# Optimization experiments

Measured on AMD Instinct MI355X. Metric: run time of the kernel, lower is better.

The kernel has to match this reference:

```python
import jax, jax.numpy as jnp
import numpy as np

G = 2000      # num_genes
TF = 64       # num_tf
B = 32        # batch (cells)
_peaks = 5 + (np.arange(G) % 46)          # ragged peaks per gene, avg ~27
T = int(_peaks.sum())                      # 54736 total peak columns
E = G * 16                                 # directed edges before symmetrization


def setup_inputs() -> dict:
    key = jax.random.key(0)
    ks = jax.random.split(key, 8)
    x = jax.random.normal(ks[0], (B, TF, T), jnp.float32)
    # gene id of each peak column (sorted, ragged segment structure = cut[])
    gene_ids = jnp.asarray(np.repeat(np.arange(G), _peaks), jnp.int32)
    # all per-gene subNet Linear weights flattened into one [TF, T] table
    w_sub = jax.random.normal(ks[1], (TF, T), jnp.float32) * 0.02
    b_sub = jax.random.normal(ks[2], (G,), jnp.float32) * 0.02
    rng = np.random.default_rng(1)
    src = rng.integers(0, G, E)
    dst = rng.integers(0, G, E)
    ei = np.stack([np.concatenate([src, dst]), np.concatenate([dst, src])])
    edge_index = jnp.asarray(ei, jnp.int32)                 # [2, 2E], symmetrized
    w_conv = jax.random.normal(ks[3], (1, 2), jnp.float32) * 0.5   # GCN lin weight (in=1, out=2)
    b_conv = jax.random.normal(ks[4], (2,), jnp.float32) * 0.1
    w_out = jax.random.normal(ks[5], (G * 2, 3), jnp.float32) * 0.02
    b_out = jax.random.normal(ks[6], (3,), jnp.float32) * 0.02
    return dict(x=x, gene_ids=gene_ids, w_sub=w_sub, b_sub=b_sub,
                edge_index=edge_index, w_conv=w_conv, b_conv=b_conv,
                w_out=w_out, b_out=b_out)


def reference(x, gene_ids, w_sub, b_sub, edge_index, w_conv, b_conv, w_out, b_out):
    # --- ragged per-gene subNets: Linear(num_peak_i*TF, 1) each ---
    # out[b,g] = sum_{t, p in gene g} x[b,t,p] * w[g,t,p] + b_sub[g]
    z = (x * w_sub[None]).sum(axis=1)                        # [B, T] reduce over TF
    x_cat = jnp.zeros((x.shape[0], b_sub.shape[0]), x.dtype)
    x_cat = x_cat.at[:, gene_ids].add(z) + b_sub[None]       # segment-sum over peaks
    x_cat = jax.nn.relu(x_cat)                               # cat_activate

    # --- GCNConv(1, 2, add_self_loops=False) on node features [B, G, 1] ---
    h = jnp.einsum('bn,f->bnf', x_cat, w_conv[0])            # lin: [B, G, 2]
    src, dst = edge_index[0], edge_index[1]
    deg = jnp.zeros((b_sub.shape[0],), x.dtype).at[dst].add(1.0)
    dinv = jnp.where(deg > 0, jax.lax.rsqrt(jnp.maximum(deg, 1.0)), 0.0)
    norm = dinv[src] * dinv[dst]                             # [2E]
    msg = h[:, src, :] * norm[None, :, None]                 # gather + scale
    agg = jnp.zeros_like(h).at[:, dst, :].add(msg) + b_conv  # scatter-add + bias
    g = jax.nn.relu(agg).reshape(x.shape[0], -1)             # [B, G*2]

    out = g @ w_out + b_out                                   # [B, 3]
    return x_cat, g, out
```

## Files before the change

### kernel.cpp

```cpp
#include <hip/hip_runtime.h>


__global__ void k_subnet(const float* __restrict__ x, const float* __restrict__ w_sub,
                         const int* __restrict__ gene_ids, float* __restrict__ acc,
                         int TF, int T, int G) {
    int t = (blockIdx.x * blockDim.x + threadIdx.x) * 4;
    int b = blockIdx.y;
    if (t >= T) return;
    const size_t xbase = (size_t)b * TF * T;
    if (t + 3 < T && (T % 4) == 0) {
        const float4* xp = (const float4*)(x + xbase + t);
        const float4* wp = (const float4*)(w_sub + t);
        const size_t strideV = (size_t)T / 4;
        float4 a = make_float4(0.f, 0.f, 0.f, 0.f);
        #pragma unroll 8
        for (int tf = 0; tf < TF; ++tf) {
            float4 xv = xp[(size_t)tf * strideV];
            float4 wv = wp[(size_t)tf * strideV];
            a.x += xv.x * wv.x;
            a.y += xv.y * wv.y;
            a.z += xv.z * wv.z;
            a.w += xv.w * wv.w;
        }
        int g0 = gene_ids[t], g1 = gene_ids[t + 1], g2 = gene_ids[t + 2], g3 = gene_ids[t + 3];
        float* base = acc + (size_t)b * G;
        float v = a.x; int cg = g0;
        if (g1 == cg) v += a.y; else { atomicAdd(base + cg, v); cg = g1; v = a.y; }
        if (g2 == cg) v += a.z; else { atomicAdd(base + cg, v); cg = g2; v = a.z; }
        if (g3 == cg) v += a.w; else { atomicAdd(base + cg, v); cg = g3; v = a.w; }
        atomicAdd(base + cg, v);
    } else {
        for (int tt = t; tt < T && tt < t + 4; ++tt) {
            float a = 0.f;
            for (int tf = 0; tf < TF; ++tf)
                a += x[xbase + (size_t)tf * T + tt] * w_sub[(size_t)tf * T + tt];
            atomicAdd(acc + (size_t)b * G + gene_ids[tt], a);
        }
    }
}

__global__ void k_xcat(const float* __restrict__ acc, const float* __restrict__ b_sub,
                       float* __restrict__ xcat, int BG, int G) {
    int i = blockIdx.x * blockDim.x + threadIdx.x;
    if (i >= BG) return;
    int g = i % G;
    float v = acc[i] + b_sub[g];
    xcat[i] = v > 0.f ? v : 0.f;
}

__global__ void k_deg(const int* __restrict__ ei, float* __restrict__ deg, int E2) {
    int e = blockIdx.x * blockDim.x + threadIdx.x;
    if (e < E2) atomicAdd(&deg[ei[E2 + e]], 1.0f);
}

__global__ void k_dinv(float* __restrict__ deg, int G) {
    int g = blockIdx.x * blockDim.x + threadIdx.x;
    if (g < G) {
        float d = deg[g];
        deg[g] = (d > 0.f) ? (1.0f / sqrtf(fmaxf(d, 1.0f))) : 0.f;
    }
}

__global__ void k_scatter(const float* __restrict__ xcat, const int* __restrict__ ei,
                          const float* __restrict__ dinv, float* __restrict__ s,
                          int G, int E2, int total) {
    int idx = blockIdx.x * blockDim.x + threadIdx.x;
    if (idx >= total) return;
    int b = idx / E2;
    int e = idx - b * E2;
    int src = ei[e], dst = ei[E2 + e];
    float norm = dinv[src] * dinv[dst];
    atomicAdd(&s[(size_t)b * G + dst], xcat[(size_t)b * G + src] * norm);
}

__global__ void k_gfin(const float* __restrict__ s, const float* __restrict__ w_conv,
                       const float* __restrict__ b_conv, float* __restrict__ gout, int BG) {
    int i = blockIdx.x * blockDim.x + threadIdx.x;
    if (i >= BG) return;
    float sv = s[i];
    float g0 = sv * w_conv[0] + b_conv[0];
    float g1 = sv * w_conv[1] + b_conv[1];
    gout[2 * (size_t)i + 0] = g0 > 0.f ? g0 : 0.f;
    gout[2 * (size_t)i + 1] = g1 > 0.f ? g1 : 0.f;
}

__global__ void k_out(const float* __restrict__ gmat, const float* __restrict__ w_out,
                      const float* __restrict__ b_out, float* __restrict__ out, int G2) {
    int b = blockIdx.x;
    float a0 = 0.f, a1 = 0.f, a2 = 0.f;
    for (int i = threadIdx.x; i < G2; i += blockDim.x) {
        float gv = gmat[(size_t)b * G2 + i];
        a0 += gv * w_out[3 * i + 0];
        a1 += gv * w_out[3 * i + 1];
        a2 += gv * w_out[3 * i + 2];
    }
    __shared__ float red[3][256];
    red[0][threadIdx.x] = a0; red[1][threadIdx.x] = a1; red[2][threadIdx.x] = a2;
    __syncthreads();
    for (int s = blockDim.x / 2; s > 0; s >>= 1) {
        if ((int)threadIdx.x < s) {
            red[0][threadIdx.x] += red[0][threadIdx.x + s];
            red[1][threadIdx.x] += red[1][threadIdx.x + s];
            red[2][threadIdx.x] += red[2][threadIdx.x + s];
        }
        __syncthreads();
    }
    if (threadIdx.x == 0) {
        out[b * 3 + 0] = red[0][0] + b_out[0];
        out[b * 3 + 1] = red[1][0] + b_out[1];
        out[b * 3 + 2] = red[2][0] + b_out[2];
    }
}

extern "C" void kernel_launch(void* const* d_in, const int* in_sizes, int n_in,
                              void* d_out, int out_size, void* d_ws, size_t ws_size,
                              hipStream_t stream) {
    const float* x        = (const float*)d_in[0];
    const int*   gene_ids = (const int*)d_in[1];
    const float* w_sub    = (const float*)d_in[2];
    const float* b_sub    = (const float*)d_in[3];
    const int*   ei       = (const int*)d_in[4];
    const float* w_conv   = (const float*)d_in[5];
    const float* b_conv   = (const float*)d_in[6];
    const float* w_out    = (const float*)d_in[7];
    const float* b_out    = (const float*)d_in[8];

    const int G  = in_sizes[3];
    const int T  = in_sizes[1];
    const int TF = in_sizes[2] / T;
    const int B  = in_sizes[0] / (TF * T);
    const int E2 = in_sizes[4] / 2;
    const int BG = B * G;
    const int G2 = 2 * G;

    float* acc = (float*)d_ws;
    float* deg = acc + BG;
    float* s   = deg + G;
    size_t zero_bytes = (size_t)(BG + G + BG) * sizeof(float);
    hipMemsetAsync(d_ws, 0, zero_bytes, stream);

    float* out_xcat = (float*)d_out;
    float* out_g    = out_xcat + BG;
    float* out_fin  = out_g + (size_t)B * G2;

    {
        int tthreads = (T + 3) / 4;
        dim3 grid((tthreads + 255) / 256, B);
        k_subnet<<<grid, 256, 0, stream>>>(x, w_sub, gene_ids, acc, TF, T, G);
    }
    k_xcat<<<(BG + 255) / 256, 256, 0, stream>>>(acc, b_sub, out_xcat, BG, G);
    k_deg<<<(E2 + 255) / 256, 256, 0, stream>>>(ei, deg, E2);
    k_dinv<<<(G + 255) / 256, 256, 0, stream>>>(deg, G);
    {
        int total = B * E2;
        k_scatter<<<(total + 255) / 256, 256, 0, stream>>>(out_xcat, ei, deg, s, G, E2, total);
    }
    k_gfin<<<(BG + 255) / 256, 256, 0, stream>>>(s, w_conv, b_conv, out_g, BG);
    k_out<<<B, 256, 0, stream>>>(out_g, w_out, b_out, out_fin, G2);
}
```

Baseline: 740.4 us.

## Fuse small GCN kernels, inline rsqrt norm, use nontemporal x loads

Merges xcat, degree counting and output-bias init into one kernel, folds the dinv computation into the scatter kernel, and fuses the gfin and final matvec into one kernel that reduces with wave shuffles and atomics. The subnet kernel now uses nontemporal vector loads for x and a single int4 load for gene ids. The aim is to cut launch count and intermediate round trips. In exchange it recomputes rsqrt per edge per batch and adds atomics on the output.

```diff
diff --git a/kernel.cpp b/kernel.cpp
--- a/kernel.cpp
+++ b/kernel.cpp
@@ -1,5 +1,7 @@
 #include <hip/hip_runtime.h>
 
+
+typedef float f32x4 __attribute__((ext_vector_type(4)));
 
 __global__ void k_subnet(const float* __restrict__ x, const float* __restrict__ w_sub,
                          const int* __restrict__ gene_ids, float* __restrict__ acc,
@@ -9,25 +11,22 @@
     if (t >= T) return;
     const size_t xbase = (size_t)b * TF * T;
     if (t + 3 < T && (T % 4) == 0) {
-        const float4* xp = (const float4*)(x + xbase + t);
-        const float4* wp = (const float4*)(w_sub + t);
+        const f32x4* xp = (const f32x4*)(x + xbase + t);
+        const f32x4* wp = (const f32x4*)(w_sub + t);
         const size_t strideV = (size_t)T / 4;
-        float4 a = make_float4(0.f, 0.f, 0.f, 0.f);
+        f32x4 a = {0.f, 0.f, 0.f, 0.f};
         #pragma unroll 8
         for (int tf = 0; tf < TF; ++tf) {
-            float4 xv = xp[(size_t)tf * strideV];
-            float4 wv = wp[(size_t)tf * strideV];
-            a.x += xv.x * wv.x;
-            a.y += xv.y * wv.y;
-            a.z += xv.z * wv.z;
-            a.w += xv.w * wv.w;
+            f32x4 xv = __builtin_nontemporal_load(xp + (size_t)tf * strideV);
+            f32x4 wv = wp[(size_t)tf * strideV];
+            a += xv * wv;
         }
-        int g0 = gene_ids[t], g1 = gene_ids[t + 1], g2 = gene_ids[t + 2], g3 = gene_ids[t + 3];
+        int4 gi = *(const int4*)(gene_ids + t);
         float* base = acc + (size_t)b * G;
-        float v = a.x; int cg = g0;
-        if (g1 == cg) v += a.y; else { atomicAdd(base + cg, v); cg = g1; v = a.y; }
-        if (g2 == cg) v += a.z; else { atomicAdd(base + cg, v); cg = g2; v = a.z; }
-        if (g3 == cg) v += a.w; else { atomicAdd(base + cg, v); cg = g3; v = a.w; }
+        float v = a.x; int cg = gi.x;
+        if (gi.y == cg) v += a.y; else { atomicAdd(base + cg, v); cg = gi.y; v = a.y; }
+        if (gi.z == cg) v += a.z; else { atomicAdd(base + cg, v); cg = gi.z; v = a.z; }
+        if (gi.w == cg) v += a.w; else { atomicAdd(base + cg, v); cg = gi.w; v = a.w; }
         atomicAdd(base + cg, v);
     } else {
         for (int tt = t; tt < T && tt < t + 4; ++tt) {
@@ -39,76 +38,66 @@
     }
 }
 
-__global__ void k_xcat(const float* __restrict__ acc, const float* __restrict__ b_sub,
-                       float* __restrict__ xcat, int BG, int G) {
+__global__ void k_xcatdeg(const float* __restrict__ acc, const float* __restrict__ b_sub,
+                          float* __restrict__ xcat,
+                          const int* __restrict__ ei, float* __restrict__ deg,
+                          const float* __restrict__ b_out, float* __restrict__ out_fin,
+                          int BG, int G, int E2, int B3) {
     int i = blockIdx.x * blockDim.x + threadIdx.x;
-    if (i >= BG) return;
-    int g = i % G;
-    float v = acc[i] + b_sub[g];
-    xcat[i] = v > 0.f ? v : 0.f;
-}
-
-__global__ void k_deg(const int* __restrict__ ei, float* __restrict__ deg, int E2) {
-    int e = blockIdx.x * blockDim.x + threadIdx.x;
-    if (e < E2) atomicAdd(&deg[ei[E2 + e]], 1.0f);
-}
-
-__global__ void k_dinv(float* __restrict__ deg, int G) {
-    int g = blockIdx.x * blockDim.x + threadIdx.x;
-    if (g < G) {
-        float d = deg[g];
-        deg[g] = (d > 0.f) ? (1.0f / sqrtf(fmaxf(d, 1.0f))) : 0.f;
+    if (i < BG) {
+        int g = i % G;
+        float v = acc[i] + b_sub[g];
+        xcat[i] = v > 0.f ? v : 0.f;
     }
+    if (i < E2) atomicAdd(&deg[ei[E2 + i]], 1.0f);
+    if (i < B3) out_fin[i] = b_out[i % 3];
 }
 
 __global__ void k_scatter(const float* __restrict__ xcat, const int* __restrict__ ei,
-                          const float* __restrict__ dinv, float* __restrict__ s,
-                          int G, int E2, int total) {
-    int idx = blockIdx.x * blockDim.x + threadIdx.x;
-    if (idx >= total) return;
-    int b = idx / E2;
-    int e = idx - b * E2;
+                          const float* __restrict__ deg, float* __restrict__ s,
+                          int G, int E2) {
+    int e = blockIdx.x * blockDim.x + threadIdx.x;
+    if (e >= E2) return;
+    int b = blockIdx.y;
     int src = ei[e], dst = ei[E2 + e];
-    float norm = dinv[src] * dinv[dst];
-    atomicAdd(&s[(size_t)b * G + dst], xcat[(size_t)b * G + src] * norm);
+    float ds = deg[src], dd = deg[dst];
+    float ns = (ds > 0.f) ? (1.0f / sqrtf(fmaxf(ds, 1.0f))) : 0.f;
+    float nd = (dd > 0.f) ? (1.0f / sqrtf(fmaxf(dd, 1.0f))) : 0.f;
+    atomicAdd(&s[(size_t)b * G + dst], xcat[(size_t)b * G + src] * (ns * nd));
 }
 
-__global__ void k_gfin(const float* __restrict__ s, const float* __restrict__ w_conv,
-                       const float* __restrict__ b_conv, float* __restrict__ gout, int BG) {
-    int i = blockIdx.x * blockDim.x + threadIdx.x;
-    if (i >= BG) return;
-    float sv = s[i];
-    float g0 = sv * w_conv[0] + b_conv[0];
-    float g1 = sv * w_conv[1] + b_conv[1];
-    gout[2 * (size_t)i + 0] = g0 > 0.f ? g0 : 0.f;
-    gout[2 * (size_t)i + 1] = g1 > 0.f ? g1 : 0.f;
-}
-
-__global__ void k_out(const float* __restrict__ gmat, const float* __restrict__ w_out,
-                      const float* __restrict__ b_out, float* __restrict__ out, int G2) {
-    int b = blockIdx.x;
+__global__ void k_gfinout(const float* __restrict__ s, const float* __restrict__ w_conv,
+                          const float* __restrict__ b_conv, const float* __restrict__ w_out,
+                          float* __restrict__ gout, float* __restrict__ out_fin, int G) {
+    int n = blockIdx.x * blockDim.x + threadIdx.x;
+    int b = blockIdx.y;
     float a0 = 0.f, a1 = 0.f, a2 = 0.f;
-    for (int i = threadIdx.x; i < G2; i += blockDim.x) {
-        float gv = gmat[(size_t)b * G2 + i];
-        a0 += gv * w_out[3 * i + 0];
-        a1 += gv * w_out[3 * i + 1];
-        a2 += gv * w_out[3 * i + 2];
+    if (n < G) {
+        size_t i = (size_t)b * G + n;
+        float sv = s[i];
+        float g0 = sv * w_conv[0] + b_conv[0]; g0 = g0 > 0.f ? g0 : 0.f;
+        float g1 = sv * w_conv[1] + b_conv[1]; g1 = g1 > 0.f ? g1 : 0.f;
+        gout[2 * i + 0] = g0;
+        gout[2 * i + 1] = g1;
+        const float* w0 = w_out + (size_t)6 * n;
+        a0 = g0 * w0[0] + g1 * w0[3];
+        a1 = g0 * w0[1] + g1 * w0[4];
+        a2 = g0 * w0[2] + g1 * w0[5];
     }
-    __shared__ float red[3][256];
-    red[0][threadIdx.x] = a0; red[1][threadIdx.x] = a1; red[2][threadIdx.x] = a2;
+    for (int off = 32; off > 0; off >>= 1) {
+        a0 += __shfl_down(a0, off);
+        a1 += __shfl_down(a1, off);
+        a2 += __shfl_down(a2, off);
+    }
+    __shared__ float red[3][4];
+    int lane = threadIdx.x & 63;
+    int wid  = threadIdx.x >> 6;
+    if (lane == 0) { red[0][wid] = a0; red[1][wid] = a1; red[2][wid] = a2; }
     __syncthreads();
-    for (int s = blockDim.x / 2; s > 0; s >>= 1) {
-        if ((int)threadIdx.x < s) {
-            red[0][threadIdx.x] += red[0][threadIdx.x + s];
-            red[1][threadIdx.x] += red[1][threadIdx.x + s];
-            red[2][threadIdx.x] += red[2][threadIdx.x + s];
-        }
-        __syncthreads();
-    }
     if (threadIdx.x == 0) {
-        out[b * 3 + 0] = red[0][0] + b_out[0];
-        out[b * 3 + 1] = red[1][0] + b_out[1];
-        out[b * 3 + 2] = red[2][0] + b_out[2];
+        atomicAdd(&out_fin[b * 3 + 0], red[0][0] + red[0][1] + red[0][2] + red[0][3]);
+        atomicAdd(&out_fin[b * 3 + 1], red[1][0] + red[1][1] + red[1][2] + red[1][3]);
+        atomicAdd(&out_fin[b * 3 + 2], red[2][0] + red[2][1] + red[2][2] + red[2][3]);
     }
 }
 
@@ -131,30 +120,34 @@
     const int B  = in_sizes[0] / (TF * T);
     const int E2 = in_sizes[4] / 2;
     const int BG = B * G;
-    const int G2 = 2 * G;
 
     float* acc = (float*)d_ws;
     float* deg = acc + BG;
     float* s   = deg + G;
-    size_t zero_bytes = (size_t)(BG + G + BG) * sizeof(float);
-    hipMemsetAsync(d_ws, 0, zero_bytes, stream);
+    hipMemsetAsync(d_ws, 0, (size_t)(BG + G + BG) * sizeof(float), stream);
 
     float* out_xcat = (float*)d_out;
     float* out_g    = out_xcat + BG;
-    float* out_fin  = out_g + (size_t)B * G2;
+    float* out_fin  = out_g + (size_t)2 * BG;
 
     {
         int tthreads = (T + 3) / 4;
         dim3 grid((tthreads + 255) / 256, B);
         k_subnet<<<grid, 256, 0, stream>>>(x, w_sub, gene_ids, acc, TF, T, G);
     }
-    k_xcat<<<(BG + 255) / 256, 256, 0, stream>>>(acc, b_sub, out_xcat, BG, G);
-    k_deg<<<(E2 + 255) / 256, 256, 0, stream>>>(ei, deg, E2);
-    k_dinv<<<(G + 255) / 256, 256, 0, stream>>>(deg, G);
     {
-        int total = B * E2;
-        k_scatter<<<(total + 255) / 256, 256, 0, stream>>>(out_xcat, ei, deg, s, G, E2, total);
+        int mx = BG > E2 ? BG : E2;
+        int b3 = B * 3;
+        if (mx < b3) mx = b3;
+        k_xcatdeg<<<(mx + 255) / 256, 256, 0, stream>>>(acc, b_sub, out_xcat, ei, deg,
+                                                        b_out, out_fin, BG, G, E2, b3);
     }
-    k_gfin<<<(BG + 255) / 256, 256, 0, stream>>>(s, w_conv, b_conv, out_g, BG);
-    k_out<<<B, 256, 0, stream>>>(out_g, w_out, b_out, out_fin, G2);
+    {
+        dim3 grid((E2 + 255) / 256, B);
+        k_scatter<<<grid, 256, 0, stream>>>(out_xcat, ei, deg, s, G, E2);
+    }
+    {
+        dim3 grid((G + 255) / 256, B);
+        k_gfinout<<<grid, 256, 0, stream>>>(s, w_conv, b_conv, w_out, out_g, out_fin, G);
+    }
 }
```

New measurement: 722.5 us, median of 2. 2.4% less time.
